# Optimization experiments

Measured on AMD Instinct MI355X. Metric: run time of the kernel, lower is better.

Reference implementation:

```python
import jax, jax.numpy as jnp
import numpy as np

B, M, P, W = 128, 10000, 64, 24


def setup_inputs() -> dict:
    key = jax.random.key(0)
    k1, k2, k3 = jax.random.split(key, 3)
    x = jax.random.normal(k1, (B, M, P), dtype=jnp.float32)
    weight = jax.random.normal(k2, (M, P, W), dtype=jnp.float32)
    bound = 1.0 / np.sqrt(P)
    bias = jax.random.uniform(k3, (M, W), dtype=jnp.float32, minval=-bound, maxval=bound)
    return {"x": x, "weight": weight, "bias": bias}


def reference(x, weight, bias):
    # Per-channel linear: out[b, w, j] = sum_p x[b, j, p] * weight[j, p, w] + bias[j, w]
    # Replaces the original python loop of m tiny GEMMs with one batched contraction.
    out = jnp.einsum('bjp,jpw->bwj', x, weight) + bias.T[None, :, :]  # [B, W, M]
    return out
```

## Files before the change

### kernel.cpp

```cpp
#include <hip/hip_runtime.h>


constexpr int B  = 128;
constexpr int M  = 10000;
constexpr int P  = 64;
constexpr int W  = 24;

constexpr int JT  = 16;
constexpr int BH  = 32;
constexpr int NT  = 512;
constexpr int NWG = (M / JT) * (B / BH);

using bf8   = __attribute__((ext_vector_type(8))) __bf16;
using f32x4 = __attribute__((ext_vector_type(4))) float;

__global__ __launch_bounds__(NT, 4) void pcl_kernel(
    const float* __restrict__ x, const float* __restrict__ wgt,
    const float* __restrict__ bias, float* __restrict__ out) {
  __shared__ __align__(16) char smem[49152];
  unsigned short* wsh  = reinterpret_cast<unsigned short*>(smem);
  float*          obuf = reinterpret_cast<float*>(smem);

  const int t = threadIdx.x;

  const int orig = blockIdx.x;
  const int xcd  = orig & 7;
  const int idx  = orig >> 3;
  const int wgid = (xcd < 4 ? xcd * 313 : 1252 + (xcd - 4) * 312) + idx;
  const int jt = wgid >> 2;
  const int by = wgid & 3;
  const int j0 = jt * JT;
  const int b0 = by * BH;

  {
    const float4* wg4 = reinterpret_cast<const float4*>(wgt);
#pragma unroll
    for (int i = 0; i < 12; ++i) {
      const int s  = t + i * NT;
      const int j  = s / 384;
      const int rr = s - j * 384;
      const int p  = rr / 6;
      const int w4 = (rr - 6 * p) * 4;
      const float4 v = wg4[(size_t)(j0 + j) * 384 + rr];
      const float vv[4] = {v.x, v.y, v.z, v.w};
#pragma unroll
      for (int k = 0; k < 4; ++k) {
        const int w = w4 + k;
        const unsigned u = __float_as_uint(vv[k]);
        const unsigned short h =
            (unsigned short)((u + 0x7fffu + ((u >> 16) & 1u)) >> 16);
        wsh[((j * W + w) << 6) + (((p >> 3) ^ (w & 7)) << 3) + (p & 7)] = h;
      }
    }
  }

  const int wk   = t >> 6;
  const int lane = t & 63;
  const int col  = lane & 15;
  const int kg   = lane >> 4;

  f32x4 acc[2][2][2];
#pragma unroll
  for (int jj = 0; jj < 2; ++jj) {
    const int j = j0 + wk + 8 * jj;
#pragma unroll
    for (int nt = 0; nt < 2; ++nt) {
      const int w  = nt * 16 + col;
      const float bv = (w < W) ? bias[(size_t)j * W + w] : 0.0f;
#pragma unroll
      for (int mt = 0; mt < 2; ++mt) acc[jj][mt][nt] = f32x4{bv, bv, bv, bv};
    }
  }

  __syncthreads();

#pragma unroll
  for (int jj = 0; jj < 2; ++jj) {
    const int jl = wk + 8 * jj;
    const int j  = j0 + jl;
#pragma unroll
    for (int ks = 0; ks < 2; ++ks) {
      bf8 af[2];
#pragma unroll
      for (int mt = 0; mt < 2; ++mt) {
        const float* xr =
            x + ((size_t)(b0 + mt * 16 + col) * M + j) * P + ks * 32 + kg * 8;
        const float4 u0 = *reinterpret_cast<const float4*>(xr);
        const float4 u1 = *reinterpret_cast<const float4*>(xr + 4);
        af[mt][0] = (__bf16)u0.x; af[mt][1] = (__bf16)u0.y;
        af[mt][2] = (__bf16)u0.z; af[mt][3] = (__bf16)u0.w;
        af[mt][4] = (__bf16)u1.x; af[mt][5] = (__bf16)u1.y;
        af[mt][6] = (__bf16)u1.z; af[mt][7] = (__bf16)u1.w;
      }
      bf8 bfr[2];
#pragma unroll
      for (int nt = 0; nt < 2; ++nt) {
        const int w  = nt * 16 + col;
        const int wr = (w < W) ? w : 0;
        const int c  = ks * 4 + kg;
        bf8 v = *reinterpret_cast<const bf8*>(
            wsh + ((jl * W + wr) << 6) + ((c ^ (wr & 7)) << 3));
        if (w >= W) {
#pragma unroll
          for (int e = 0; e < 8; ++e) v[e] = (__bf16)0.0f;
        }
        bfr[nt] = v;
      }
#pragma unroll
      for (int mt = 0; mt < 2; ++mt)
#pragma unroll
        for (int nt = 0; nt < 2; ++nt)
          acc[jj][mt][nt] = __builtin_amdgcn_mfma_f32_16x16x32_bf16(
              af[mt], bfr[nt], acc[jj][mt][nt], 0, 0, 0);
    }
  }

  __syncthreads();
#pragma unroll
  for (int r = 0; r < 2; ++r) {
#pragma unroll
    for (int jj = 0; jj < 2; ++jj) {
      const int jl = wk + 8 * jj;
#pragma unroll
      for (int nt = 0; nt < 2; ++nt) {
        const int w = nt * 16 + col;
        if (w < W) {
#pragma unroll
          for (int reg = 0; reg < 4; ++reg) {
            const int brow = kg * 4 + reg;
            obuf[(jl * 16 + brow) * 25 + w] = acc[jj][r][nt][reg];
          }
        }
      }
    }
    __syncthreads();
#pragma unroll
    for (int it = 0; it < 3; ++it) {
      const int d    = t + it * NT;
      const int jq   = d & 3;
      const int rest = d >> 2;
      const int w    = rest % 24;
      const int br   = rest / 24;
      float4 o;
      o.x = obuf[((4 * jq + 0) * 16 + br) * 25 + w];
      o.y = obuf[((4 * jq + 1) * 16 + br) * 25 + w];
      o.z = obuf[((4 * jq + 2) * 16 + br) * 25 + w];
      o.w = obuf[((4 * jq + 3) * 16 + br) * 25 + w];
      *reinterpret_cast<float4*>(
          out + ((size_t)(b0 + r * 16 + br) * W + w) * M + j0 + 4 * jq) = o;
    }
    if (r == 0) __syncthreads();
  }
}

extern "C" void kernel_launch(void* const* d_in, const int* in_sizes, int n_in,
                              void* d_out, int out_size, void* d_ws, size_t ws_size,
                              hipStream_t stream) {
  const float* x    = (const float*)d_in[0];
  const float* wgt  = (const float*)d_in[1];
  const float* bias = (const float*)d_in[2];
  float* out        = (float*)d_out;

  dim3 grid(NWG);
  dim3 block(NT);
  hipLaunchKernelGGL(pcl_kernel, grid, block, 0, stream, x, wgt, bias, out);
}
```

Before: 130.1 us.

## Halve batch tile and stage x through swizzled LDS with coalesced loads

The batch tile per workgroup drops from 32 to 16 rows, which doubles the grid and reloads each weight tile twice as often. x is now loaded cooperatively with coalesced float4 reads, converted to bf16 and stored in a swizzled LDS buffer, replacing the per-lane strided global reads of MFMA fragments. The XCD-aware block remapping is simplified to a uniform split, and the epilogue handles one 16-row pass instead of two. LDS use grows to 80KB per block, which may limit occupancy, and total weight traffic and bf16 conversion work double.

```diff
diff --git a/kernel.cpp b/kernel.cpp
--- a/kernel.cpp
+++ b/kernel.cpp
@@ -7,28 +7,32 @@
 constexpr int W  = 24;
 
 constexpr int JT  = 16;
-constexpr int BH  = 32;
+constexpr int BH  = 16;
 constexpr int NT  = 512;
 constexpr int NWG = (M / JT) * (B / BH);
 
 using bf8   = __attribute__((ext_vector_type(8))) __bf16;
 using f32x4 = __attribute__((ext_vector_type(4))) float;
 
+__device__ __forceinline__ unsigned short rne_bf16(float f) {
+  const unsigned u = __float_as_uint(f);
+  return (unsigned short)((u + 0x7fffu + ((u >> 16) & 1u)) >> 16);
+}
+
 __global__ __launch_bounds__(NT, 4) void pcl_kernel(
     const float* __restrict__ x, const float* __restrict__ wgt,
     const float* __restrict__ bias, float* __restrict__ out) {
-  __shared__ __align__(16) char smem[49152];
+  __shared__ __align__(16) char smem[81920];
   unsigned short* wsh  = reinterpret_cast<unsigned short*>(smem);
+  unsigned short* xsh  = reinterpret_cast<unsigned short*>(smem + 49152);
   float*          obuf = reinterpret_cast<float*>(smem);
 
   const int t = threadIdx.x;
 
   const int orig = blockIdx.x;
-  const int xcd  = orig & 7;
-  const int idx  = orig >> 3;
-  const int wgid = (xcd < 4 ? xcd * 313 : 1252 + (xcd - 4) * 312) + idx;
-  const int jt = wgid >> 2;
-  const int by = wgid & 3;
+  const int wgid = (orig & 7) * (NWG / 8) + (orig >> 3);
+  const int jt = wgid >> 3;
+  const int by = wgid & 7;
   const int j0 = jt * JT;
   const int b0 = by * BH;
 
@@ -46,11 +50,28 @@
 #pragma unroll
       for (int k = 0; k < 4; ++k) {
         const int w = w4 + k;
-        const unsigned u = __float_as_uint(vv[k]);
-        const unsigned short h =
-            (unsigned short)((u + 0x7fffu + ((u >> 16) & 1u)) >> 16);
-        wsh[((j * W + w) << 6) + (((p >> 3) ^ (w & 7)) << 3) + (p & 7)] = h;
+        wsh[((j * W + w) << 6) + (((p >> 3) ^ (w & 7)) << 3) + (p & 7)] =
+            rne_bf16(vv[k]);
       }
+    }
+  }
+
+  {
+#pragma unroll
+    for (int i = 0; i < 8; ++i) {
+      const int g   = t + i * NT;
+      const int b   = g >> 8;
+      const int rem = g & 255;
+      const int j   = rem >> 4;
+      const int c2  = rem & 15;
+      const float4 v = *reinterpret_cast<const float4*>(
+          x + ((size_t)(b0 + b) * M + j0 + j) * P + 4 * c2);
+      const unsigned u0 = (unsigned)rne_bf16(v.x) | ((unsigned)rne_bf16(v.y) << 16);
+      const unsigned u1 = (unsigned)rne_bf16(v.z) | ((unsigned)rne_bf16(v.w) << 16);
+      const int s = (c2 >> 1) ^ (b & 7);
+      uint2* dst = reinterpret_cast<uint2*>(
+          xsh + (((b << 4) + j) << 6) + (s << 3) + ((c2 & 1) << 2));
+      *dst = uint2{u0, u1};
     }
   }
 
@@ -59,16 +80,15 @@
   const int col  = lane & 15;
   const int kg   = lane >> 4;
 
-  f32x4 acc[2][2][2];
+  f32x4 acc[2][2];
 #pragma unroll
   for (int jj = 0; jj < 2; ++jj) {
     const int j = j0 + wk + 8 * jj;
 #pragma unroll
     for (int nt = 0; nt < 2; ++nt) {
-      const int w  = nt * 16 + col;
+      const int w = nt * 16 + col;
       const float bv = (w < W) ? bias[(size_t)j * W + w] : 0.0f;
-#pragma unroll
-      for (int mt = 0; mt < 2; ++mt) acc[jj][mt][nt] = f32x4{bv, bv, bv, bv};
+      acc[jj][nt] = f32x4{bv, bv, bv, bv};
     }
   }
 
@@ -77,27 +97,16 @@
 #pragma unroll
   for (int jj = 0; jj < 2; ++jj) {
     const int jl = wk + 8 * jj;
-    const int j  = j0 + jl;
 #pragma unroll
     for (int ks = 0; ks < 2; ++ks) {
-      bf8 af[2];
-#pragma unroll
-      for (int mt = 0; mt < 2; ++mt) {
-        const float* xr =
-            x + ((size_t)(b0 + mt * 16 + col) * M + j) * P + ks * 32 + kg * 8;
-        const float4 u0 = *reinterpret_cast<const float4*>(xr);
-        const float4 u1 = *reinterpret_cast<const float4*>(xr + 4);
-        af[mt][0] = (__bf16)u0.x; af[mt][1] = (__bf16)u0.y;
-        af[mt][2] = (__bf16)u0.z; af[mt][3] = (__bf16)u0.w;
-        af[mt][4] = (__bf16)u1.x; af[mt][5] = (__bf16)u1.y;
-        af[mt][6] = (__bf16)u1.z; af[mt][7] = (__bf16)u1.w;
-      }
+      const int c = ks * 4 + kg;
+      const bf8 af = *reinterpret_cast<const bf8*>(
+          xsh + (((col << 4) + jl) << 6) + ((c ^ (col & 7)) << 3));
       bf8 bfr[2];
 #pragma unroll
       for (int nt = 0; nt < 2; ++nt) {
         const int w  = nt * 16 + col;
         const int wr = (w < W) ? w : 0;
-        const int c  = ks * 4 + kg;
         bf8 v = *reinterpret_cast<const bf8*>(
             wsh + ((jl * W + wr) << 6) + ((c ^ (wr & 7)) << 3));
         if (w >= W) {
@@ -107,49 +116,43 @@
         bfr[nt] = v;
       }
 #pragma unroll
-      for (int mt = 0; mt < 2; ++mt)
-#pragma unroll
-        for (int nt = 0; nt < 2; ++nt)
-          acc[jj][mt][nt] = __builtin_amdgcn_mfma_f32_16x16x32_bf16(
-              af[mt], bfr[nt], acc[jj][mt][nt], 0, 0, 0);
+      for (int nt = 0; nt < 2; ++nt)
+        acc[jj][nt] = __builtin_amdgcn_mfma_f32_16x16x32_bf16(
+            af, bfr[nt], acc[jj][nt], 0, 0, 0);
     }
   }
 
   __syncthreads();
 #pragma unroll
-  for (int r = 0; r < 2; ++r) {
+  for (int jj = 0; jj < 2; ++jj) {
+    const int jl = wk + 8 * jj;
 #pragma unroll
-    for (int jj = 0; jj < 2; ++jj) {
-      const int jl = wk + 8 * jj;
+    for (int nt = 0; nt < 2; ++nt) {
+      const int w = nt * 16 + col;
+      if (w < W) {
 #pragma unroll
-      for (int nt = 0; nt < 2; ++nt) {
-        const int w = nt * 16 + col;
-        if (w < W) {
-#pragma unroll
-          for (int reg = 0; reg < 4; ++reg) {
-            const int brow = kg * 4 + reg;
-            obuf[(jl * 16 + brow) * 25 + w] = acc[jj][r][nt][reg];
-          }
+        for (int reg = 0; reg < 4; ++reg) {
+          const int brow = kg * 4 + reg;
+          obuf[(jl * 16 + brow) * 25 + w] = acc[jj][nt][reg];
         }
       }
     }
-    __syncthreads();
+  }
+  __syncthreads();
 #pragma unroll
-    for (int it = 0; it < 3; ++it) {
-      const int d    = t + it * NT;
-      const int jq   = d & 3;
-      const int rest = d >> 2;
-      const int w    = rest % 24;
-      const int br   = rest / 24;
-      float4 o;
-      o.x = obuf[((4 * jq + 0) * 16 + br) * 25 + w];
-      o.y = obuf[((4 * jq + 1) * 16 + br) * 25 + w];
-      o.z = obuf[((4 * jq + 2) * 16 + br) * 25 + w];
-      o.w = obuf[((4 * jq + 3) * 16 + br) * 25 + w];
-      *reinterpret_cast<float4*>(
-          out + ((size_t)(b0 + r * 16 + br) * W + w) * M + j0 + 4 * jq) = o;
-    }
-    if (r == 0) __syncthreads();
+  for (int it = 0; it < 3; ++it) {
+    const int d    = t + it * NT;
+    const int jq   = d & 3;
+    const int rest = d >> 2;
+    const int w    = rest % 24;
+    const int br   = rest / 24;
+    float4 o;
+    o.x = obuf[((4 * jq + 0) * 16 + br) * 25 + w];
+    o.y = obuf[((4 * jq + 1) * 16 + br) * 25 + w];
+    o.z = obuf[((4 * jq + 2) * 16 + br) * 25 + w];
+    o.w = obuf[((4 * jq + 3) * 16 + br) * 25 + w];
+    *reinterpret_cast<float4*>(
+        out + ((size_t)(b0 + br) * W + w) * M + j0 + 4 * jq) = o;
   }
 }
 
```

After: 125.6 us. 1.04x faster.
